# Kernel tuning notes

Measured on AMD Instinct MI355X. Metric: run time of the kernel, lower is better.

## Reference

```python
import jax, jax.numpy as jnp
import numpy as np

N_NODES = 50000
N_EDGES = 800000
D_IN = 512
D_OUT = 128

def setup_inputs() -> dict:
    key = jax.random.key(0)
    k1, k2, k3, k4, k5, k6 = jax.random.split(key, 6)
    std = 1.0 / np.sqrt(D_OUT)
    x = jax.random.normal(k1, (N_NODES, D_IN), dtype=jnp.float32)
    edge_w = jax.random.uniform(k2, (N_EDGES,), dtype=jnp.float32)
    src = jax.random.randint(k3, (N_EDGES,), 0, N_NODES, dtype=jnp.int32)
    dst = jax.random.randint(k4, (N_EDGES,), 0, N_NODES, dtype=jnp.int32)
    W = jax.random.uniform(k5, (D_IN, D_OUT), minval=-std, maxval=std, dtype=jnp.float32)
    b = jax.random.uniform(k6, (D_OUT,), minval=-std, maxval=std, dtype=jnp.float32)
    return {"x": x, "edge_w": edge_w, "src": src, "dst": dst, "W": W, "b": b}

def reference(x, edge_w, src, dst, W, b):
    # Dense GEMM: [N, D_in] @ [D_in, D_out]
    h = x @ W
    # SpMM with COO adjacency: out[i] = sum_{e: dst[e]==i} edge_w[e] * h[src[e]]
    msg = h[src] * edge_w[:, None]          # [E, D_out]
    agg = jax.ops.segment_sum(msg, dst, num_segments=N_NODES)
    return agg + b
```

## Files before the change

kernel.cpp:

```cpp
#include <hip/hip_runtime.h>
#include <hip/hip_bf16.h>

#define M_NODES  50000
#define D_IN_K   512
#define D_OUT_N  128
#define N_EDGES  800000
#define SCAN_NBLK 49

typedef short  bf16x8 __attribute__((ext_vector_type(8)));
typedef float  f32x4  __attribute__((ext_vector_type(4)));

static __device__ __forceinline__ unsigned short f2bf(float f) {
    unsigned u = __float_as_uint(f);
    unsigned r = u + 0x7FFF + ((u >> 16) & 1);
    return (unsigned short)(r >> 16);
}
static __device__ __forceinline__ float bflo(unsigned q) { return __uint_as_float(q << 16); }
static __device__ __forceinline__ float bfhi(unsigned q) { return __uint_as_float(q & 0xFFFF0000u); }

static __device__ __forceinline__ void gl2lds16(const uint4* g, uint4* l) {
    __builtin_amdgcn_global_load_lds(
        (const __attribute__((address_space(1))) void*)g,
        (__attribute__((address_space(3))) void*)l,
        16, 0, 0);
}

__global__ __launch_bounds__(256) void permw_kernel(const float* __restrict__ W,
                                                    unsigned short* __restrict__ Wp,
                                                    int* __restrict__ counts) {
    int tid = blockIdx.x * 256 + threadIdx.x;
    int lane = tid & 63;
    int nt   = (tid >> 6) & 7;
    int kb4  = tid >> 9;
    int n    = nt * 16 + (lane & 15);
    int kbase = kb4 * 32 + ((lane >> 4) & 3) * 8;
    unsigned short frag[8];
#pragma unroll
    for (int j = 0; j < 8; ++j)
        frag[j] = f2bf(W[(size_t)(kbase + j) * D_OUT_N + n]);
    *(uint4*)&Wp[(size_t)tid * 8] = *(const uint4*)frag;

    for (int i = tid; i < M_NODES + 64; i += 8192) counts[i] = 0;
}

__global__ __launch_bounds__(512, 4) void mfma_gemm_hist_kernel(const float* __restrict__ x,
                                                                const uint4* __restrict__ Wp4,
                                                                unsigned short* __restrict__ h,
                                                                const int* __restrict__ dst,
                                                                int* __restrict__ counts,
                                                                int* __restrict__ rank) {
    __shared__ uint4 wlds[4096];

    const int tid  = threadIdx.x;
    const int wave = tid >> 6;
    const int lane = tid & 63;
    const int m0   = blockIdx.x * 128 + wave * 16;
    const int mrow = lane & 15;
    const int kgrp = lane >> 4;

    const int r0 = m0 + mrow;
    const float* xr0 = x + (size_t)((r0 < M_NODES) ? r0 : M_NODES - 1) * D_IN_K + kgrp * 8;

    f32x4 acc[8];
#pragma unroll
    for (int t = 0; t < 8; ++t) acc[t] = (f32x4){0.f, 0.f, 0.f, 0.f};

    for (int half = 0; half < 2; ++half) {
        __syncthreads();
#pragma unroll
        for (int i = 0; i < 8; ++i)
            gl2lds16(Wp4 + half * 4096 + tid + i * 512, &wlds[tid + i * 512]);

        const float* px0 = xr0 + half * 256;
        float4 ax[16];
#pragma unroll
        for (int kb = 0; kb < 8; ++kb) {
            ax[2 * kb]     = *(const float4*)(px0 + kb * 32);
            ax[2 * kb + 1] = *(const float4*)(px0 + kb * 32 + 4);
        }

        __syncthreads();

#pragma unroll
        for (int kb = 0; kb < 8; ++kb) {
            union { bf16x8 v; __hip_bfloat162 h2[4]; } c0;
            c0.h2[0] = __float22bfloat162_rn(make_float2(ax[2 * kb].x, ax[2 * kb].y));
            c0.h2[1] = __float22bfloat162_rn(make_float2(ax[2 * kb].z, ax[2 * kb].w));
            c0.h2[2] = __float22bfloat162_rn(make_float2(ax[2 * kb + 1].x, ax[2 * kb + 1].y));
            c0.h2[3] = __float22bfloat162_rn(make_float2(ax[2 * kb + 1].z, ax[2 * kb + 1].w));
            bf16x8 a0 = c0.v;

#pragma unroll
            for (int nt = 0; nt < 8; ++nt) {
                union { uint4 u; bf16x8 v; } wb;
                wb.u = wlds[(kb * 8 + nt) * 64 + lane];
                acc[nt] = __builtin_amdgcn_mfma_f32_16x16x32_bf16(a0, wb.v, acc[nt], 0, 0, 0);
            }
        }
    }

#pragma unroll
    for (int r = 0; r < 4; ++r) {
        int rr = m0 + kgrp * 4 + r;
        if (rr < M_NODES) {
            unsigned short* hp = h + (size_t)rr * D_OUT_N + mrow;
#pragma unroll
            for (int nt = 0; nt < 8; ++nt)
                hp[nt * 16] = f2bf(acc[nt][r]);
        }
    }

    const int epb = (N_EDGES + gridDim.x - 1) / gridDim.x;
    const int e0  = blockIdx.x * epb;
    const int e1  = (e0 + epb < N_EDGES) ? e0 + epb : N_EDGES;
    for (int e = e0 + tid; e < e1; e += 512)
        rank[e] = atomicAdd(&counts[dst[e]], 1);
}

__global__ __launch_bounds__(256) void scan_kernel(const int* __restrict__ counts,
                                                   int* __restrict__ offsets,
                                                   int* __restrict__ partials,
                                                   int* __restrict__ flags) {
    __shared__ int wsum[4];
    __shared__ int carry_s;
    const int tid  = threadIdx.x;
    const int lane = tid & 63;
    const int wid  = tid >> 6;
    const int blk  = blockIdx.x;
    const int base = blk * 1024 + tid * 4;

    int v[4];
    if (base + 3 < M_NODES) {
        int4 q = *(const int4*)&counts[base];
        v[0] = q.x; v[1] = q.y; v[2] = q.z; v[3] = q.w;
    } else {
#pragma unroll
        for (int i = 0; i < 4; ++i)
            v[i] = (base + i < M_NODES) ? counts[base + i] : 0;
    }
    int t = v[0] + v[1] + v[2] + v[3];

    int s = t;
#pragma unroll
    for (int d = 1; d < 64; d <<= 1) {
        int u = __shfl_up(s, d, 64);
        if (lane >= d) s += u;
    }
    if (lane == 63) wsum[wid] = s;
    __syncthreads();
    int wbase = 0;
#pragma unroll
    for (int w = 0; w < 4; ++w) wbase += (w < wid) ? wsum[w] : 0;
    int total = wsum[0] + wsum[1] + wsum[2] + wsum[3];

    if (tid == 0) {
        __hip_atomic_store(&partials[blk], total, __ATOMIC_RELAXED, __HIP_MEMORY_SCOPE_AGENT);
        __hip_atomic_store(&flags[blk], 1, __ATOMIC_RELEASE, __HIP_MEMORY_SCOPE_AGENT);
        if (blk == 0) offsets[M_NODES] = N_EDGES;
    }

    if (wid == 0) {
        int val = 0;
        if (lane < blk) {
            while (__hip_atomic_load(&flags[lane], __ATOMIC_ACQUIRE, __HIP_MEMORY_SCOPE_AGENT) == 0) {}
            val = __hip_atomic_load(&partials[lane], __ATOMIC_RELAXED, __HIP_MEMORY_SCOPE_AGENT);
        }
#pragma unroll
        for (int d = 32; d > 0; d >>= 1) val += __shfl_xor(val, d, 64);
        if (lane == 0) carry_s = val;
    }
    __syncthreads();
    const int carry = carry_s;

    int run = carry + wbase + s - t;
#pragma unroll
    for (int i = 0; i < 4; ++i) {
        if (base + i < M_NODES) offsets[base + i] = run;
        run += v[i];
    }
}

__global__ __launch_bounds__(256) void fill_kernel(const int* __restrict__ src,
                                                   const int* __restrict__ dst,
                                                   const float* __restrict__ edge_w,
                                                   const int* __restrict__ rank,
                                                   const int* __restrict__ offsets,
                                                   int2* __restrict__ ep) {
    int base = (blockIdx.x * 256 + threadIdx.x) * 4;
    if (base >= N_EDGES) return;
    int4   s4 = *(const int4*)&src[base];
    int4   d4 = *(const int4*)&dst[base];
    int4   r4 = *(const int4*)&rank[base];
    float4 w4 = *(const float4*)&edge_w[base];
    ep[offsets[d4.x] + r4.x] = make_int2(s4.x, __float_as_int(w4.x));
    ep[offsets[d4.y] + r4.y] = make_int2(s4.y, __float_as_int(w4.y));
    ep[offsets[d4.z] + r4.z] = make_int2(s4.z, __float_as_int(w4.z));
    ep[offsets[d4.w] + r4.w] = make_int2(s4.w, __float_as_int(w4.w));
}

__global__ __launch_bounds__(256) void gather_kernel(const unsigned short* __restrict__ h,
                                                     const int2* __restrict__ ep,
                                                     const int* __restrict__ offsets,
                                                     const float* __restrict__ b,
                                                     float* __restrict__ out) {
    int t    = blockIdx.x * blockDim.x + threadIdx.x;
    int node = t >> 4;
    int lane = t & 15;
    if (node >= M_NODES) return;
    int beg = offsets[node];
    int end = offsets[node + 1];

    float4 b0 = *(const float4*)&b[lane * 8];
    float4 b1 = *(const float4*)&b[lane * 8 + 4];
    float a[4][8];
#pragma unroll
    for (int u = 0; u < 4; ++u)
#pragma unroll
        for (int c = 0; c < 8; ++c) a[u][c] = 0.f;

    int j = beg;
    for (; j + 4 <= end; j += 4) {
        int2 e0 = ep[j], e1 = ep[j + 1], e2 = ep[j + 2], e3 = ep[j + 3];
        uint4 q0 = *(const uint4*)(h + (size_t)e0.x * D_OUT_N + lane * 8);
        uint4 q1 = *(const uint4*)(h + (size_t)e1.x * D_OUT_N + lane * 8);
        uint4 q2 = *(const uint4*)(h + (size_t)e2.x * D_OUT_N + lane * 8);
        uint4 q3 = *(const uint4*)(h + (size_t)e3.x * D_OUT_N + lane * 8);
        float w0 = __int_as_float(e0.y), w1 = __int_as_float(e1.y);
        float w2 = __int_as_float(e2.y), w3 = __int_as_float(e3.y);
        a[0][0] += w0 * bflo(q0.x);  a[0][1] += w0 * bfhi(q0.x);
        a[0][2] += w0 * bflo(q0.y);  a[0][3] += w0 * bfhi(q0.y);
        a[0][4] += w0 * bflo(q0.z);  a[0][5] += w0 * bfhi(q0.z);
        a[0][6] += w0 * bflo(q0.w);  a[0][7] += w0 * bfhi(q0.w);
        a[1][0] += w1 * bflo(q1.x);  a[1][1] += w1 * bfhi(q1.x);
        a[1][2] += w1 * bflo(q1.y);  a[1][3] += w1 * bfhi(q1.y);
        a[1][4] += w1 * bflo(q1.z);  a[1][5] += w1 * bfhi(q1.z);
        a[1][6] += w1 * bflo(q1.w);  a[1][7] += w1 * bfhi(q1.w);
        a[2][0] += w2 * bflo(q2.x);  a[2][1] += w2 * bfhi(q2.x);
        a[2][2] += w2 * bflo(q2.y);  a[2][3] += w2 * bfhi(q2.y);
        a[2][4] += w2 * bflo(q2.z);  a[2][5] += w2 * bfhi(q2.z);
        a[2][6] += w2 * bflo(q2.w);  a[2][7] += w2 * bfhi(q2.w);
        a[3][0] += w3 * bflo(q3.x);  a[3][1] += w3 * bfhi(q3.x);
        a[3][2] += w3 * bflo(q3.y);  a[3][3] += w3 * bfhi(q3.y);
        a[3][4] += w3 * bflo(q3.z);  a[3][5] += w3 * bfhi(q3.z);
        a[3][6] += w3 * bflo(q3.w);  a[3][7] += w3 * bfhi(q3.w);
    }
    for (; j < end; ++j) {
        int2 e0 = ep[j];
        float w0 = __int_as_float(e0.y);
        uint4 q0 = *(const uint4*)(h + (size_t)e0.x * D_OUT_N + lane * 8);
        a[0][0] += w0 * bflo(q0.x);  a[0][1] += w0 * bfhi(q0.x);
        a[0][2] += w0 * bflo(q0.y);  a[0][3] += w0 * bfhi(q0.y);
        a[0][4] += w0 * bflo(q0.z);  a[0][5] += w0 * bfhi(q0.z);
        a[0][6] += w0 * bflo(q0.w);  a[0][7] += w0 * bfhi(q0.w);
    }

    float4 o0 = make_float4(b0.x + a[0][0] + a[1][0] + a[2][0] + a[3][0],
                            b0.y + a[0][1] + a[1][1] + a[2][1] + a[3][1],
                            b0.z + a[0][2] + a[1][2] + a[2][2] + a[3][2],
                            b0.w + a[0][3] + a[1][3] + a[2][3] + a[3][3]);
    float4 o1 = make_float4(b1.x + a[0][4] + a[1][4] + a[2][4] + a[3][4],
                            b1.y + a[0][5] + a[1][5] + a[2][5] + a[3][5],
                            b1.z + a[0][6] + a[1][6] + a[2][6] + a[3][6],
                            b1.w + a[0][7] + a[1][7] + a[2][7] + a[3][7]);
    float* op = &out[(size_t)node * D_OUT_N + lane * 8];
    *(float4*)op = o0;
    *(float4*)(op + 4) = o1;
}

extern "C" void kernel_launch(void* const* d_in, const int* in_sizes, int n_in,
                              void* d_out, int out_size, void* d_ws, size_t ws_size,
                              hipStream_t stream) {
    const float* x      = (const float*)d_in[0];
    const float* edge_w = (const float*)d_in[1];
    const int*   src    = (const int*)d_in[2];
    const int*   dst    = (const int*)d_in[3];
    const float* W      = (const float*)d_in[4];
    const float* b      = (const float*)d_in[5];
    float* out = (float*)d_out;

    char* wsp = (char*)d_ws;
    unsigned short* h = (unsigned short*)wsp;  wsp += (size_t)M_NODES * D_OUT_N * 2;
    int*   counts   = (int*)wsp;         wsp += (size_t)M_NODES * 4;
    int*   flags    = (int*)wsp;         wsp += 64 * 4;
    int*   offsets  = (int*)wsp;         wsp += (((size_t)M_NODES + 1) * 4 + 15) & ~15ull;
    int*   rank     = (int*)wsp;         wsp += (size_t)N_EDGES * 4;
    int2*  ep       = (int2*)wsp;        wsp += (size_t)N_EDGES * 8;
    unsigned short* Wp = (unsigned short*)wsp; wsp += (size_t)16 * 8 * 64 * 8 * 2;
    int*   partials = (int*)wsp;         wsp += (SCAN_NBLK * 4 + 15) & ~15ull;

    permw_kernel<<<32, 256, 0, stream>>>(W, Wp, counts);
    mfma_gemm_hist_kernel<<<(M_NODES + 127) / 128, 512, 0, stream>>>(
        x, (const uint4*)Wp, h, dst, counts, rank);
    scan_kernel<<<SCAN_NBLK, 256, 0, stream>>>(counts, offsets, partials, flags);
    fill_kernel<<<(N_EDGES / 4 + 255) / 256, 256, 0, stream>>>(src, dst, edge_w, rank, offsets, ep);
    gather_kernel<<<(int)(((long long)M_NODES * 16 + 255) / 256), 256, 0, stream>>>(
        h, ep, offsets, b, out);
}
```

Measured before the change: 253.0 us.

## Overlap dst histogram atomics with second-half GEMM loads using vectorized edge access

```diff
diff --git a/kernel.cpp b/kernel.cpp
--- a/kernel.cpp
+++ b/kernel.cpp
@@ -58,6 +58,11 @@
     const int mrow = lane & 15;
     const int kgrp = lane >> 4;
 
+    const int ebase = (blockIdx.x * 512 + tid) * 4;
+    const bool edo = ebase < N_EDGES;
+    int4 d4 = make_int4(0, 0, 0, 0);
+    if (edo) d4 = *(const int4*)&dst[ebase];
+
     const int r0 = m0 + mrow;
     const float* xr0 = x + (size_t)((r0 < M_NODES) ? r0 : M_NODES - 1) * D_IN_K + kgrp * 8;
 
@@ -65,37 +70,68 @@
 #pragma unroll
     for (int t = 0; t < 8; ++t) acc[t] = (f32x4){0.f, 0.f, 0.f, 0.f};
 
-    for (int half = 0; half < 2; ++half) {
-        __syncthreads();
-#pragma unroll
-        for (int i = 0; i < 8; ++i)
-            gl2lds16(Wp4 + half * 4096 + tid + i * 512, &wlds[tid + i * 512]);
-
-        const float* px0 = xr0 + half * 256;
-        float4 ax[16];
-#pragma unroll
-        for (int kb = 0; kb < 8; ++kb) {
-            ax[2 * kb]     = *(const float4*)(px0 + kb * 32);
-            ax[2 * kb + 1] = *(const float4*)(px0 + kb * 32 + 4);
+    float4 ax[16];
+
+#pragma unroll
+    for (int i = 0; i < 8; ++i)
+        gl2lds16(Wp4 + tid + i * 512, &wlds[tid + i * 512]);
+#pragma unroll
+    for (int kb = 0; kb < 8; ++kb) {
+        ax[2 * kb]     = *(const float4*)(xr0 + kb * 32);
+        ax[2 * kb + 1] = *(const float4*)(xr0 + kb * 32 + 4);
+    }
+    __syncthreads();
+
+#pragma unroll
+    for (int kb = 0; kb < 8; ++kb) {
+        union { bf16x8 v; __hip_bfloat162 h2[4]; } c0;
+        c0.h2[0] = __float22bfloat162_rn(make_float2(ax[2 * kb].x, ax[2 * kb].y));
+        c0.h2[1] = __float22bfloat162_rn(make_float2(ax[2 * kb].z, ax[2 * kb].w));
+        c0.h2[2] = __float22bfloat162_rn(make_float2(ax[2 * kb + 1].x, ax[2 * kb + 1].y));
+        c0.h2[3] = __float22bfloat162_rn(make_float2(ax[2 * kb + 1].z, ax[2 * kb + 1].w));
+        bf16x8 a0 = c0.v;
+#pragma unroll
+        for (int nt = 0; nt < 8; ++nt) {
+            union { uint4 u; bf16x8 v; } wb;
+            wb.u = wlds[(kb * 8 + nt) * 64 + lane];
+            acc[nt] = __builtin_amdgcn_mfma_f32_16x16x32_bf16(a0, wb.v, acc[nt], 0, 0, 0);
         }
-
-        __syncthreads();
-
-#pragma unroll
-        for (int kb = 0; kb < 8; ++kb) {
-            union { bf16x8 v; __hip_bfloat162 h2[4]; } c0;
-            c0.h2[0] = __float22bfloat162_rn(make_float2(ax[2 * kb].x, ax[2 * kb].y));
-            c0.h2[1] = __float22bfloat162_rn(make_float2(ax[2 * kb].z, ax[2 * kb].w));
-            c0.h2[2] = __float22bfloat162_rn(make_float2(ax[2 * kb + 1].x, ax[2 * kb + 1].y));
-            c0.h2[3] = __float22bfloat162_rn(make_float2(ax[2 * kb + 1].z, ax[2 * kb + 1].w));
-            bf16x8 a0 = c0.v;
-
-#pragma unroll
-            for (int nt = 0; nt < 8; ++nt) {
-                union { uint4 u; bf16x8 v; } wb;
-                wb.u = wlds[(kb * 8 + nt) * 64 + lane];
-                acc[nt] = __builtin_amdgcn_mfma_f32_16x16x32_bf16(a0, wb.v, acc[nt], 0, 0, 0);
-            }
+    }
+
+    __syncthreads();
+#pragma unroll
+    for (int i = 0; i < 8; ++i)
+        gl2lds16(Wp4 + 4096 + tid + i * 512, &wlds[tid + i * 512]);
+    const float* px1 = xr0 + 256;
+#pragma unroll
+    for (int kb = 0; kb < 8; ++kb) {
+        ax[2 * kb]     = *(const float4*)(px1 + kb * 32);
+        ax[2 * kb + 1] = *(const float4*)(px1 + kb * 32 + 4);
+    }
+    int4 r4 = make_int4(0, 0, 0, 0);
+    if (edo) {
+        r4.x = atomicAdd(&counts[d4.x], 1);
+        r4.y = atomicAdd(&counts[d4.y], 1);
+        r4.z = atomicAdd(&counts[d4.z], 1);
+        r4.w = atomicAdd(&counts[d4.w], 1);
+    }
+    asm volatile("s_waitcnt vmcnt(4)" ::: "memory");
+    __builtin_amdgcn_sched_barrier(0);
+    __builtin_amdgcn_s_barrier();
+
+#pragma unroll
+    for (int kb = 0; kb < 8; ++kb) {
+        union { bf16x8 v; __hip_bfloat162 h2[4]; } c0;
+        c0.h2[0] = __float22bfloat162_rn(make_float2(ax[2 * kb].x, ax[2 * kb].y));
+        c0.h2[1] = __float22bfloat162_rn(make_float2(ax[2 * kb].z, ax[2 * kb].w));
+        c0.h2[2] = __float22bfloat162_rn(make_float2(ax[2 * kb + 1].x, ax[2 * kb + 1].y));
+        c0.h2[3] = __float22bfloat162_rn(make_float2(ax[2 * kb + 1].z, ax[2 * kb + 1].w));
+        bf16x8 a0 = c0.v;
+#pragma unroll
+        for (int nt = 0; nt < 8; ++nt) {
+            union { uint4 u; bf16x8 v; } wb;
+            wb.u = wlds[(kb * 8 + nt) * 64 + lane];
+            acc[nt] = __builtin_amdgcn_mfma_f32_16x16x32_bf16(a0, wb.v, acc[nt], 0, 0, 0);
         }
     }
 
@@ -110,11 +146,7 @@
         }
     }
 
-    const int epb = (N_EDGES + gridDim.x - 1) / gridDim.x;
-    const int e0  = blockIdx.x * epb;
-    const int e1  = (e0 + epb < N_EDGES) ? e0 + epb : N_EDGES;
-    for (int e = e0 + tid; e < e1; e += 512)
-        rank[e] = atomicAdd(&counts[dst[e]], 1);
+    if (edo) *(int4*)&rank[ebase] = r4;
 }
 
 __global__ __launch_bounds__(256) void scan_kernel(const int* __restrict__ counts,
```

Measured after the change: 249.4 us. Within noise of the previous version (-1.4%).
